# Optimization experiments

Hardware: AMD Instinct MI355X
Metric: run time of the kernel (lower is better)

The kernel has to match this reference:

```python
import jax, jax.numpy as jnp
import numpy as np

HEADS = 8
DIM_HEAD = 64
SCALE = DIM_HEAD ** (-0.5)


def _flatten_like_module(t):
    # Reproduces: jnp.transpose(t, (0,2,1,3)).reshape(t.shape[0], t.shape[1], t.shape[2]*t.shape[3])
    # where the reshape dims come from the ORIGINAL (pre-transpose) shape.
    B, S, H, Dh = t.shape
    return jnp.transpose(t, (0, 2, 1, 3)).reshape(B, S, H * Dh)


def _heads_to_batch(t):
    b, s, d = t.shape
    t = t.reshape(b, s, HEADS, d // HEADS)
    t = jnp.transpose(t, (0, 2, 1, 3))
    return t.reshape(b * HEADS, s, d // HEADS)


def setup_inputs() -> dict:
    key = jax.random.key(0)
    kq, kk, kv = jax.random.split(key, 3)
    shape = (2, 16384, 8, 64)  # [B, S, heads, dim_head]
    return {
        "query": jax.random.normal(kq, shape, dtype=jnp.float32),
        "key": jax.random.normal(kk, shape, dtype=jnp.float32),
        "value": jax.random.normal(kv, shape, dtype=jnp.float32),
    }


def reference(query, key, value):
    q = _heads_to_batch(_flatten_like_module(query))   # [B*H, S, Dh]
    k = _heads_to_batch(_flatten_like_module(key))     # [B*H, S, Dh]
    # Swapped contraction: reduce over the sequence axis -> [B*H, Dh, Dh]
    scores = jnp.einsum('bdi,bdj->bij', q, k) * SCALE
    probs = jax.nn.softmax(scores, axis=2)
    v = _heads_to_batch(_flatten_like_module(value))   # [B*H, S, Dh]
    # NOTE: computed in the original module but never returned (dead under jit DCE)
    _hidden = jnp.einsum('bij,bdj->bid', probs, v)     # [B*H, Dh, S]
    return probs
```

## Files before the change

### kernel.cpp

```cpp
#include <hip/hip_runtime.h>
#include <hip/hip_bf16.h>

#define NB 2
#define NS 16384
#define NH 8
#define ND 64
#define BUCKETS 16
#define ROW_FLOATS 512

__device__ __forceinline__ void gload_lds16(const float* g, float* l) {
    __builtin_amdgcn_global_load_lds(
        (const __attribute__((address_space(1))) void*)g,
        (__attribute__((address_space(3))) void*)l,
        16 , 0 , 0 );
}

__global__ __launch_bounds__(256) void gram_partial(
    const float* __restrict__ Q, const float* __restrict__ K,
    float* __restrict__ part, int bpb, int shi_per_blk)
{
    const int bid    = blockIdx.x;
    const int bucket = bid / bpb;
    const int chunk  = bid % bpb;
    const int b      = bucket >> 3;
    const int r      = bucket & 7;

    const int tid  = threadIdx.x;
    const int lane = tid & 63;
    const int wv   = tid >> 6;
    const int ty   = tid >> 4;
    const int tx   = tid & 15;

    __shared__ __align__(16) float sbuf[2][2 * ROW_FLOATS];

    float acc[4][4] = {};

    const float* gten = (wv >= 2 ? K : Q) + (size_t)b * ((size_t)NS * ROW_FLOATS);
    const int half = (wv & 1);
    float* l0 = &sbuf[0][(wv >= 2 ? ROW_FLOATS : 0) + half * 256];
    float* l1 = &sbuf[1][(wv >= 2 ? ROW_FLOATS : 0) + half * 256];

    const int s0 = chunk * shi_per_blk;
    const float* gcur = gten + ((size_t)s0 * 4096 + (size_t)r * ROW_FLOATS
                                + half * 256 + lane * 4);
    const size_t gstep = 4096;

    gload_lds16(gcur, l0);

    for (int c = 0; c < shi_per_blk; ++c) {
        if (c + 1 < shi_per_blk) {
            gload_lds16(gcur + gstep, (c & 1) ? l0 : l1);
        }
        gcur += gstep;
        __syncthreads();

        const float* bq = &sbuf[c & 1][0];
        const float* bk = &sbuf[c & 1][ROW_FLOATS];
        #pragma unroll
        for (int tr = 0; tr < 8; ++tr) {
            const float4 qv = *(const float4*)(bq + tr * 64 + ty * 4);
            const float4 kv = *(const float4*)(bk + tr * 64 + tx * 4);
            const float qa[4] = {qv.x, qv.y, qv.z, qv.w};
            const float ka[4] = {kv.x, kv.y, kv.z, kv.w};
            #pragma unroll
            for (int ii = 0; ii < 4; ++ii)
                #pragma unroll
                for (int jj = 0; jj < 4; ++jj)
                    acc[ii][jj] += qa[ii] * ka[jj];
        }
        __syncthreads();
    }

    float* p = part + (size_t)bid * 4096;
    #pragma unroll
    for (int ii = 0; ii < 4; ++ii) {
        float4 v = make_float4(acc[ii][0], acc[ii][1], acc[ii][2], acc[ii][3]);
        *(float4*)(p + (ty * 4 + ii) * 64 + tx * 4) = v;
    }
}

__global__ __launch_bounds__(256) void reduce_softmax(
    const float* __restrict__ part, float* __restrict__ out, int bpb)
{
    const int g   = blockIdx.x >> 4;
    const int cg  = blockIdx.x & 15;
    const int tid = threadIdx.x;
    const int e   = cg * 256 + tid;

    const float* p = part + (size_t)g * bpb * 4096 + e;
    float s = 0.f;
    for (int k = 0; k < bpb; ++k) s += p[(size_t)k * 4096];
    s *= 0.125f;

    float m = s;
    #pragma unroll
    for (int o = 32; o; o >>= 1) m = fmaxf(m, __shfl_xor(m, o));
    const float ex = __expf(s - m);
    float sum = ex;
    #pragma unroll
    for (int o = 32; o; o >>= 1) sum += __shfl_xor(sum, o);

    out[(size_t)g * 4096 + e] = ex / sum;
}

extern "C" void kernel_launch(void* const* d_in, const int* in_sizes, int n_in,
                              void* d_out, int out_size, void* d_ws, size_t ws_size,
                              hipStream_t stream)
{
    const float* Q = (const float*)d_in[0];
    const float* K = (const float*)d_in[1];
    float* out  = (float*)d_out;
    float* part = (float*)d_ws;

    int bpb = 64;
    while ((size_t)BUCKETS * bpb * 4096 * sizeof(float) > ws_size && bpb > 1) bpb >>= 1;
    const int shi_per_blk = 2048 / bpb;

    gram_partial<<<dim3(BUCKETS * bpb), dim3(256), 0, stream>>>(Q, K, part, bpb, shi_per_blk);
    reduce_softmax<<<dim3(256), dim3(256), 0, stream>>>(part, out, bpb);
}
```

Baseline: 204.5 us.

## Stage four sequence rows per LDS buffer and parallelize partial reduction

The Gram kernel now loads four sequence positions per stage (each wave loads one row of Q and K), so each double-buffered iteration covers 32 reduction rows instead of 8. The trailing barrier is removed, leaving one barrier per iteration for four times the work. The goal is to cut barrier and issue overhead per FLOP and to keep more loads in flight. The reduce kernel splits the partial-sum loop across four wave slices with an LDS combine and launches four times as many blocks, shortening each thread's serial accumulation chain.

```diff
diff --git a/kernel.cpp b/kernel.cpp
--- a/kernel.cpp
+++ b/kernel.cpp
@@ -1,18 +1,13 @@
 #include <hip/hip_runtime.h>
-#include <hip/hip_bf16.h>
 
-#define NB 2
 #define NS 16384
-#define NH 8
-#define ND 64
 #define BUCKETS 16
-#define ROW_FLOATS 512
 
 __device__ __forceinline__ void gload_lds16(const float* g, float* l) {
     __builtin_amdgcn_global_load_lds(
         (const __attribute__((address_space(1))) void*)g,
         (__attribute__((address_space(3))) void*)l,
-        16 , 0 , 0 );
+        16 , 0, 0);
 }
 
 __global__ __launch_bounds__(256) void gram_partial(
@@ -31,33 +26,36 @@
     const int ty   = tid >> 4;
     const int tx   = tid & 15;
 
-    __shared__ __align__(16) float sbuf[2][2 * ROW_FLOATS];
+    __shared__ __align__(16) float sbuf[2][4096];
+
+    const float* gq = Q + (size_t)b * ((size_t)NS * 512)
+                        + ((size_t)wv * 8 + r) * 512 + lane * 4;
+    const float* gk = K + (size_t)b * ((size_t)NS * 512)
+                        + ((size_t)wv * 8 + r) * 512 + lane * 4;
+    const size_t base_off = (size_t)chunk * shi_per_blk * 4096;
+
+    const int niter = shi_per_blk >> 2;
+
+    auto stage = [&](int it, int bufi) {
+        const size_t off = base_off + (size_t)it * 16384;
+        float* dq = &sbuf[bufi][wv * 512];
+        float* dk = &sbuf[bufi][2048 + wv * 512];
+        gload_lds16(gq + off, dq);
+        gload_lds16(gq + off + 256, dq + 256);
+        gload_lds16(gk + off, dk);
+        gload_lds16(gk + off + 256, dk + 256);
+    };
 
     float acc[4][4] = {};
 
-    const float* gten = (wv >= 2 ? K : Q) + (size_t)b * ((size_t)NS * ROW_FLOATS);
-    const int half = (wv & 1);
-    float* l0 = &sbuf[0][(wv >= 2 ? ROW_FLOATS : 0) + half * 256];
-    float* l1 = &sbuf[1][(wv >= 2 ? ROW_FLOATS : 0) + half * 256];
-
-    const int s0 = chunk * shi_per_blk;
-    const float* gcur = gten + ((size_t)s0 * 4096 + (size_t)r * ROW_FLOATS
-                                + half * 256 + lane * 4);
-    const size_t gstep = 4096;
-
-    gload_lds16(gcur, l0);
-
-    for (int c = 0; c < shi_per_blk; ++c) {
-        if (c + 1 < shi_per_blk) {
-            gload_lds16(gcur + gstep, (c & 1) ? l0 : l1);
-        }
-        gcur += gstep;
+    stage(0, 0);
+    for (int it = 0; it < niter; ++it) {
         __syncthreads();
-
-        const float* bq = &sbuf[c & 1][0];
-        const float* bk = &sbuf[c & 1][ROW_FLOATS];
+        if (it + 1 < niter) stage(it + 1, (it + 1) & 1);
+        const float* bq = &sbuf[it & 1][0];
+        const float* bk = &sbuf[it & 1][2048];
         #pragma unroll
-        for (int tr = 0; tr < 8; ++tr) {
+        for (int tr = 0; tr < 32; ++tr) {
             const float4 qv = *(const float4*)(bq + tr * 64 + ty * 4);
             const float4 kv = *(const float4*)(bk + tr * 64 + tx * 4);
             const float qa[4] = {qv.x, qv.y, qv.z, qv.w};
@@ -68,7 +66,6 @@
                 for (int jj = 0; jj < 4; ++jj)
                     acc[ii][jj] += qa[ii] * ka[jj];
         }
-        __syncthreads();
     }
 
     float* p = part + (size_t)bid * 4096;
@@ -80,27 +77,34 @@
 }
 
 __global__ __launch_bounds__(256) void reduce_softmax(
-    const float* __restrict__ part, float* __restrict__ out, int bpb)
+    const float* __restrict__ part, float* __restrict__ out, int slices)
 {
-    const int g   = blockIdx.x >> 4;
-    const int cg  = blockIdx.x & 15;
-    const int tid = threadIdx.x;
-    const int e   = cg * 256 + tid;
+    const int g   = blockIdx.x >> 6;
+    const int row = blockIdx.x & 63;
+    const int c   = threadIdx.x & 63;
+    const int sl  = threadIdx.x >> 6;
 
-    const float* p = part + (size_t)g * bpb * 4096 + e;
+    const float* p = part + (size_t)(g * (slices * 4) + sl * slices) * 4096
+                          + row * 64 + c;
     float s = 0.f;
-    for (int k = 0; k < bpb; ++k) s += p[(size_t)k * 4096];
-    s *= 0.125f;
+    #pragma unroll 4
+    for (int k = 0; k < slices; ++k) s += p[(size_t)k * 4096];
 
-    float m = s;
-    #pragma unroll
-    for (int o = 32; o; o >>= 1) m = fmaxf(m, __shfl_xor(m, o));
-    const float ex = __expf(s - m);
-    float sum = ex;
-    #pragma unroll
-    for (int o = 32; o; o >>= 1) sum += __shfl_xor(sum, o);
-
-    out[(size_t)g * 4096 + e] = ex / sum;
+    __shared__ float red[4][64];
+    red[sl][c] = s;
+    __syncthreads();
+    if (sl == 0) {
+        float v = (red[0][c] + red[1][c]) + (red[2][c] + red[3][c]);
+        v *= 0.125f;
+        float m = v;
+        #pragma unroll
+        for (int o = 32; o; o >>= 1) m = fmaxf(m, __shfl_xor(m, o));
+        const float e = __expf(v - m);
+        float sum = e;
+        #pragma unroll
+        for (int o = 32; o; o >>= 1) sum += __shfl_xor(sum, o);
+        out[(size_t)g * 4096 + row * 64 + c] = e / sum;
+    }
 }
 
 extern "C" void kernel_launch(void* const* d_in, const int* in_sizes, int n_in,
@@ -113,9 +117,9 @@
     float* part = (float*)d_ws;
 
     int bpb = 64;
-    while ((size_t)BUCKETS * bpb * 4096 * sizeof(float) > ws_size && bpb > 1) bpb >>= 1;
+    while ((size_t)BUCKETS * bpb * 4096 * sizeof(float) > ws_size && bpb > 4) bpb >>= 1;
     const int shi_per_blk = 2048 / bpb;
 
     gram_partial<<<dim3(BUCKETS * bpb), dim3(256), 0, stream>>>(Q, K, part, bpb, shi_per_blk);
-    reduce_softmax<<<dim3(256), dim3(256), 0, stream>>>(part, out, bpb);
+    reduce_softmax<<<dim3(1024), dim3(256), 0, stream>>>(part, out, bpb / 4);
 }
```

New measurement: 189.4 us. -7.4%, faster.
